# Kernel tuning notes

Hardware: AMD Instinct MI355X
Metric: run time of the kernel (lower is better)

Reference implementation:

```python
import jax, jax.numpy as jnp
import numpy as np

FEATURES = 64
GROUPS = 8
KH = KW = 3
PAD = 1


def conv2d(x, w):
    # x: [B,C,H,W], w: [O,I,kh,kw], stride 1, padding 1
    return jax.lax.conv_general_dilated(
        x, w, window_strides=(1, 1), padding=((PAD, PAD), (PAD, PAD)),
        dimension_numbers=('NCHW', 'OIHW', 'NCHW'))


def _bilinear_gather(x, ys, xs):
    # x: [B,C,H,W]; ys, xs: [B,K,H,W] float sample coords. Zero outside bounds
    # (torchvision deform_conv2d convention).
    B, C, H, W = x.shape
    xf = x.reshape(B, C, H * W)
    y0 = jnp.floor(ys)
    x0 = jnp.floor(xs)
    dy = ys - y0
    dx = xs - x0

    def corner(yi, xi, w):
        valid = (yi >= 0) & (yi < H) & (xi >= 0) & (xi < W)
        yc = jnp.clip(yi, 0, H - 1).astype(jnp.int32)
        xc = jnp.clip(xi, 0, W - 1).astype(jnp.int32)
        idx = (yc * W + xc).reshape(B, -1)  # [B, K*H*W]
        g = jax.vmap(lambda xb, ib: xb[:, ib])(xf, idx)  # [B,C,K*H*W]
        g = g.reshape(B, C, *ys.shape[1:])  # [B,C,K,H,W]
        wm = jnp.where(valid, w, 0.0).astype(x.dtype)[:, None]
        return g * wm

    return (corner(y0, x0, (1 - dy) * (1 - dx))
            + corner(y0, x0 + 1, (1 - dy) * dx)
            + corner(y0 + 1, x0, dy * (1 - dx))
            + corner(y0 + 1, x0 + 1, dy * dx))


def deform_conv2d(x, offset, weight, bias, groups):
    # x: [B,C,H,W]; offset: [B,2*K,H,W] as (dy,dx) pairs per kernel tap;
    # weight: [Cout, Cin//groups, KH, KW]; bias: [Cout]. stride=1, pad=1, dil=1.
    B, C, H, W = x.shape
    Cout = weight.shape[0]
    K = KH * KW
    ky, kx = jnp.meshgrid(jnp.arange(KH), jnp.arange(KW), indexing='ij')
    ky = ky.reshape(K).astype(x.dtype)
    kx = kx.reshape(K).astype(x.dtype)
    off = offset.reshape(B, K, 2, H, W)
    ys = ((jnp.arange(H, dtype=x.dtype) - PAD)[None, None, :, None]
          + ky[None, :, None, None] + off[:, :, 0])  # [B,K,H,W]
    xs = ((jnp.arange(W, dtype=x.dtype) - PAD)[None, None, None, :]
          + kx[None, :, None, None] + off[:, :, 1])
    patches = _bilinear_gather(x, ys, xs)  # [B,C,K,H,W]
    p = patches.reshape(B, groups, C // groups, K, H, W)
    wg = weight.reshape(groups, Cout // groups, C // groups, K)
    out = jnp.einsum('bgikhw,goik->bgohw', p, wg).reshape(B, Cout, H, W)
    return out + bias[None, :, None, None]


def setup_inputs() -> dict:
    key = jax.random.key(0)
    ks = jax.random.split(key, 7)
    C = FEATURES
    x = jax.random.normal(ks[0], (8, C, 128, 128), dtype=jnp.float32)
    fan = C * KH * KW
    offset_w = jax.random.normal(ks[1], (2 * KH * KW, C, KH, KW), jnp.float32) / np.sqrt(fan)
    offset_b = jax.random.normal(ks[2], (2 * KH * KW,), jnp.float32) * 0.01
    prelu_a = jnp.full((1,), 0.25, dtype=jnp.float32)
    deconv_w = jax.random.normal(ks[3], (C, C // GROUPS, KH, KW), jnp.float32) / np.sqrt((C // GROUPS) * KH * KW)
    deconv_b = jax.random.normal(ks[4], (C,), jnp.float32) * 0.01
    conv_w = jax.random.normal(ks[5], (C, C, KH, KW), jnp.float32) / np.sqrt(fan)
    return {"x": x, "offset_w": offset_w, "offset_b": offset_b,
            "prelu_a": prelu_a, "deconv_w": deconv_w, "deconv_b": deconv_b,
            "conv_w": conv_w}


def reference(x, offset_w, offset_b, prelu_a, deconv_w, deconv_b, conv_w):
    residual = x
    o = conv2d(x, offset_w) + offset_b[None, :, None, None]
    offset = jnp.where(o >= 0, o, prelu_a[0] * o)          # PReLU(offset_conv1(x))
    feat = deform_conv2d(x, offset, deconv_w, deconv_b, GROUPS)
    atten = jax.nn.softmax(conv2d(x, conv_w), axis=-1)     # softmax over W
    return atten * feat + residual
```

## Files before the change

### kernel.cpp

```cpp
#include <hip/hip_runtime.h>
#include <math.h>

#define BB 8
#define C 64
#define H 128
#define W 128
#define KO 18
#define NG 8
#define CPG 8
#define KK 9
#define HW (H * W)
#define NCO 96
#define KTOT 576
#define AROW 72
#define PROW 72

#define NB_XCL (BB * HW / 64)
#define NB_WT  (NCO * KTOT / 256)
#define NB_AWG (KK * 2 * 32 * 32 / 256)

typedef __bf16 bf16x8 __attribute__((ext_vector_type(8)));
typedef float f32x4 __attribute__((ext_vector_type(4)));
typedef unsigned int uint4v __attribute__((ext_vector_type(4)));

static __device__ __forceinline__ unsigned short f2bf(float f) {
    union { float f; unsigned u; } v; v.f = f;
    unsigned r = v.u + 0x7FFFu + ((v.u >> 16) & 1u);
    return (unsigned short)(r >> 16);
}

static __device__ __forceinline__ bf16x8 load_bf8(const unsigned short* p) {
    uint4v u = *(const uint4v*)p;
    return __builtin_bit_cast(bf16x8, u);
}
static __device__ __forceinline__ bf16x8 lds_bf8(const unsigned short* p) {
    uint4v u = *(const uint4v*)p;
    return __builtin_bit_cast(bf16x8, u);
}

static __device__ __forceinline__ float bflo(unsigned u) {
    union { unsigned u; float f; } v; v.u = u << 16; return v.f;
}
static __device__ __forceinline__ float bfhi(unsigned u) {
    union { unsigned u; float f; } v; v.u = u & 0xFFFF0000u; return v.f;
}

__global__ __launch_bounds__(256)
void prep_kernel(const float* __restrict__ x,
                 const float* __restrict__ convw,
                 const float* __restrict__ offw,
                 const float* __restrict__ dw,
                 unsigned short* __restrict__ xcl,
                 unsigned short* __restrict__ wT,
                 unsigned short* __restrict__ awg)
{
    const int blk = blockIdx.x;
    if (blk < NB_XCL) {
        const int lane = threadIdx.x & 63;
        const int cg = threadIdx.x >> 6;
        const size_t P = (size_t)blk * 64 + lane;
        const int b = (int)(P >> 14);
        const int hw = (int)(P & 16383);

        union { unsigned short s[16]; uint4v v[2]; } u;
        const float* xp = x + ((size_t)b * C + cg * 16) * HW + hw;
#pragma unroll
        for (int i = 0; i < 16; i++)
            u.s[i] = f2bf(xp[i * HW]);

        uint4v* dst = (uint4v*)(xcl + P * 64 + cg * 16);
        dst[0] = u.v[0];
        dst[1] = u.v[1];
    } else if (blk < NB_XCL + NB_WT) {
        const int i = (blk - NB_XCL) * 256 + threadIdx.x;
        const int k = i % KTOT;
        const int co = i / KTOT;
        const int t = k >> 6;
        const int ci = k & 63;
        float v = 0.f;
        if (co < 64)       v = convw[((size_t)co * C + ci) * KK + t];
        else if (co < 82)  v = offw[((size_t)(co - 64) * C + ci) * KK + t];
        wT[i] = f2bf(v);
    } else {
        const int i = (blk - NB_XCL - NB_WT) * 256 + threadIdx.x;
        const int ci = i & 31;
        const int row = (i >> 5) & 31;
        const int hf = (i >> 10) & 1;
        const int t = i >> 11;
        const int co = hf * 32 + row;
        const int cig = hf * 32 + ci;
        float v = 0.f;
        if ((co >> 3) == (cig >> 3))
            v = dw[((size_t)co * CPG + (cig & 7)) * KK + t];
        awg[i] = f2bf(v);
    }
}

static __device__ __forceinline__ void stage_tap(
    const unsigned short* __restrict__ wT, unsigned short* __restrict__ dst,
    int t, int tid)
{
#pragma unroll
    for (int c = tid; c < NCO * 8; c += 256) {
        const int row = c >> 3;
        const int col8 = (c & 7) * 8;
        *(uint4v*)(dst + row * AROW + col8) =
            *(const uint4v*)(wT + (size_t)row * KTOT + t * 64 + col8);
    }
}

static __device__ __forceinline__ void load_b(
    const unsigned short* __restrict__ xcl, int b, int h0, int col0, int qq,
    int t, bf16x8 (&dst)[2][4])
{
    const int dy = t / 3 - 1;
    const int dx = t % 3 - 1;
#pragma unroll
    for (int half = 0; half < 2; half++)
#pragma unroll
        for (int nt = 0; nt < 4; nt++) {
            const int y = h0 + (nt >> 1) + dy;
            const int xx = col0 + (nt & 1) * 16 + dx;
            const bool ok = (y >= 0) && (y < H) && (xx >= 0) && (xx < W);
            bf16x8 v = {};
            if (ok)
                v = load_bf8(xcl + (((size_t)(b * H + y) * W + xx) * 64
                                    + half * 32 + qq * 8));
            dst[half][nt] = v;
        }
}

__global__ __launch_bounds__(256, 2)
void conv_mfma_kernel(const unsigned short* __restrict__ xcl,
                      const unsigned short* __restrict__ wT,
                      const float* __restrict__ offb,
                      const float* __restrict__ prelu_a,
                      float* __restrict__ ws_offset,
                      float* __restrict__ ws_atten)
{
    __shared__ unsigned short aw[2][NCO * AROW];
    __shared__ float smax[4][2][64];
    __shared__ float ssum[4][2][64];

    const int lane = threadIdx.x & 63;
    const int q = __builtin_amdgcn_readfirstlane(threadIdx.x >> 6);
    const int m = lane & 15;
    const int qq = lane >> 4;
    const int hp = blockIdx.x & 63;
    const int b = blockIdx.x >> 6;
    const int h0 = hp * 2;

    f32x4 acc[4][6];
#pragma unroll
    for (int nt = 0; nt < 4; nt++)
#pragma unroll
        for (int mt = 0; mt < 6; mt++)
            acc[nt][mt] = (f32x4){0.f, 0.f, 0.f, 0.f};

    const int col0 = q * 32 + m;

    bf16x8 bcur[2][4], bnxt[2][4];
    stage_tap(wT, aw[0], 0, threadIdx.x);
    load_b(xcl, b, h0, col0, qq, 0, bcur);
    __syncthreads();

#pragma unroll
    for (int t = 0; t < KK; t++) {
        if (t + 1 < KK) {
            stage_tap(wT, aw[(t + 1) & 1], t + 1, threadIdx.x);
            load_b(xcl, b, h0, col0, qq, t + 1, bnxt);
        }

#pragma unroll
        for (int half = 0; half < 2; half++) {
#pragma unroll
            for (int mt = 0; mt < 6; mt++) {
                const bf16x8 afr = lds_bf8(
                    &aw[t & 1][(mt * 16 + m) * AROW + half * 32 + qq * 8]);
#pragma unroll
                for (int nt = 0; nt < 4; nt++)
                    acc[nt][mt] = __builtin_amdgcn_mfma_f32_16x16x32_bf16(
                        afr, bcur[half][nt], acc[nt][mt], 0, 0, 0);
            }
        }
        __syncthreads();

#pragma unroll
        for (int half = 0; half < 2; half++)
#pragma unroll
            for (int nt = 0; nt < 4; nt++)
                bcur[half][nt] = bnxt[half][nt];
    }

    const float a = prelu_a[0];
#pragma unroll
    for (int nt = 0; nt < 4; nt++) {
        const int wrow = h0 + (nt >> 1);
        const int wcol = col0 + (nt & 1) * 16;
#pragma unroll
        for (int r = 0; r < 4; r++) {
            const int j = qq * 4 + r;
            float v = acc[nt][4][r] + offb[j];
            v = (v >= 0.f) ? v : a * v;
            ws_offset[((size_t)(b * KO + j)) * HW + wrow * W + wcol] = v;
        }
#pragma unroll
        for (int r = 0; r < 4; r++) {
            const int j = 16 + qq * 4 + r;
            if (j < KO) {
                float v = acc[nt][5][r] + offb[j];
                v = (v >= 0.f) ? v : a * v;
                ws_offset[((size_t)(b * KO + j)) * HW + wrow * W + wcol] = v;
            }
        }
    }

    float pm[2][4][4];
#pragma unroll
    for (int rr = 0; rr < 2; rr++)
#pragma unroll
        for (int mt = 0; mt < 4; mt++)
#pragma unroll
            for (int r = 0; r < 4; r++)
                pm[rr][mt][r] = fmaxf(acc[rr * 2][mt][r], acc[rr * 2 + 1][mt][r]);
#pragma unroll
    for (int off = 1; off < 16; off <<= 1)
#pragma unroll
        for (int rr = 0; rr < 2; rr++)
#pragma unroll
            for (int mt = 0; mt < 4; mt++)
#pragma unroll
                for (int r = 0; r < 4; r++)
                    pm[rr][mt][r] = fmaxf(pm[rr][mt][r],
                                          __shfl_xor(pm[rr][mt][r], off, 64));
    if (m == 0) {
#pragma unroll
        for (int rr = 0; rr < 2; rr++)
#pragma unroll
            for (int mt = 0; mt < 4; mt++)
#pragma unroll
                for (int r = 0; r < 4; r++)
                    smax[q][rr][mt * 16 + qq * 4 + r] = pm[rr][mt][r];
    }
    __syncthreads();

    float gm[2][4][4];
#pragma unroll
    for (int rr = 0; rr < 2; rr++)
#pragma unroll
        for (int mt = 0; mt < 4; mt++)
#pragma unroll
            for (int r = 0; r < 4; r++) {
                const int co = mt * 16 + qq * 4 + r;
                gm[rr][mt][r] = fmaxf(fmaxf(smax[0][rr][co], smax[1][rr][co]),
                                      fmaxf(smax[2][rr][co], smax[3][rr][co]));
            }
    float ps[2][4][4];
#pragma unroll
    for (int rr = 0; rr < 2; rr++)
#pragma unroll
        for (int mt = 0; mt < 4; mt++)
#pragma unroll
            for (int r = 0; r < 4; r++) {
                acc[rr * 2][mt][r] = __expf(acc[rr * 2][mt][r] - gm[rr][mt][r]);
                acc[rr * 2 + 1][mt][r] = __expf(acc[rr * 2 + 1][mt][r] - gm[rr][mt][r]);
                ps[rr][mt][r] = acc[rr * 2][mt][r] + acc[rr * 2 + 1][mt][r];
            }
#pragma unroll
    for (int off = 1; off < 16; off <<= 1)
#pragma unroll
        for (int rr = 0; rr < 2; rr++)
#pragma unroll
            for (int mt = 0; mt < 4; mt++)
#pragma unroll
                for (int r = 0; r < 4; r++)
                    ps[rr][mt][r] += __shfl_xor(ps[rr][mt][r], off, 64);
    if (m == 0) {
#pragma unroll
        for (int rr = 0; rr < 2; rr++)
#pragma unroll
            for (int mt = 0; mt < 4; mt++)
#pragma unroll
                for (int r = 0; r < 4; r++)
                    ssum[q][rr][mt * 16 + qq * 4 + r] = ps[rr][mt][r];
    }
    __syncthreads();

#pragma unroll
    for (int rr = 0; rr < 2; rr++)
#pragma unroll
        for (int mt = 0; mt < 4; mt++)
#pragma unroll
            for (int r = 0; r < 4; r++) {
                const int co = mt * 16 + qq * 4 + r;
                const float rinv = 1.f / (ssum[0][rr][co] + ssum[1][rr][co]
                                          + ssum[2][rr][co] + ssum[3][rr][co]);
                float* op = ws_atten + ((size_t)(b * 64 + co)) * HW
                            + (h0 + rr) * W;
                op[col0] = acc[rr * 2][mt][r] * rinv;
                op[col0 + 16] = acc[rr * 2 + 1][mt][r] * rinv;
            }
}

__global__ __launch_bounds__(256)
void deform_mfma_kernel(const float* __restrict__ x,
                        const unsigned short* __restrict__ xcl,
                        const unsigned short* __restrict__ awg,
                        const float* __restrict__ db,
                        const float* __restrict__ ws_offset,
                        const float* __restrict__ ws_atten,
                        float* __restrict__ out)
{
    __shared__ unsigned short Pl[4 * 2 * 16 * PROW];

    const int lane = threadIdx.x & 63;
    const int wv = __builtin_amdgcn_readfirstlane(threadIdx.x >> 6);

    const int b = blockIdx.x & 7;
    const int h = (blockIdx.x >> 3) & 127;
    const int halfrow = blockIdx.x >> 10;
    const int w0 = halfrow * 64 + wv * 16;

    const int px = lane >> 2;
    const int ck = lane & 3;

    const unsigned short* xclb = xcl + (size_t)b * HW * 64;
    const float* offbase = ws_offset + (size_t)b * KO * HW + h * W + w0;
    unsigned short* const Pw0 = Pl + (wv * 2 + 0) * 16 * PROW;
    unsigned short* const Pw1 = Pl + (wv * 2 + 1) * 16 * PROW;

    f32x4 acc[4];
#pragma unroll
    for (int i = 0; i < 4; i++) acc[i] = (f32x4){0.f, 0.f, 0.f, 0.f};

    float dy = offbase[px];
    float dx = offbase[HW + px];

#pragma unroll
    for (int t = 0; t < KK; t++) {
        const int ky = t / 3;
        const int kx = t - ky * 3;

        float ndy = 0.f, ndx = 0.f;
        if (t + 1 < KK) {
            const float* ob2 = offbase + (size_t)(2 * t + 2) * HW;
            ndy = ob2[px];
            ndx = ob2[HW + px];
        }

        float wa[4];
        int oa[4];
        {
            const float ys = (float)(h - 1 + ky) + dy;
            const float xs = (float)(w0 + px - 1 + kx) + dx;
            const float y0f = floorf(ys), x0f = floorf(xs);
            const int y0 = (int)y0f, x0 = (int)x0f;
            const float fy = ys - y0f, fx = xs - x0f;
            const bool vy0 = (y0 >= 0) & (y0 < H), vy1 = (y0 + 1 >= 0) & (y0 + 1 < H);
            const bool vx0 = (x0 >= 0) & (x0 < W), vx1 = (x0 + 1 >= 0) & (x0 + 1 < W);
            wa[0] = (vy0 && vx0) ? (1.f - fy) * (1.f - fx) : 0.f;
            wa[1] = (vy0 && vx1) ? (1.f - fy) * fx : 0.f;
            wa[2] = (vy1 && vx0) ? fy * (1.f - fx) : 0.f;
            wa[3] = (vy1 && vx1) ? fy * fx : 0.f;
            const int yc0 = min(max(y0, 0), H - 1), yc1 = min(max(y0 + 1, 0), H - 1);
            const int xc0 = min(max(x0, 0), W - 1), xc1 = min(max(x0 + 1, 0), W - 1);
            oa[0] = (yc0 * W + xc0) * 64; oa[1] = (yc0 * W + xc1) * 64;
            oa[2] = (yc1 * W + xc0) * 64; oa[3] = (yc1 * W + xc1) * 64;
        }

        uint4v rA[4][2];
#pragma unroll
        for (int c = 0; c < 4; c++)
#pragma unroll
            for (int hh = 0; hh < 2; hh++)
                rA[c][hh] = *(const uint4v*)(xclb + oa[c] + ck * 16 + hh * 8);

        unsigned short* const Pwt = (t & 1) ? Pw1 : Pw0;

#pragma unroll
        for (int hh = 0; hh < 2; hh++) {
            bf16x8 pv;
#pragma unroll
            for (int d = 0; d < 4; d++) {
                const float lo = wa[0] * bflo(rA[0][hh][d]) + wa[1] * bflo(rA[1][hh][d])
                               + wa[2] * bflo(rA[2][hh][d]) + wa[3] * bflo(rA[3][hh][d]);
                const float hi = wa[0] * bfhi(rA[0][hh][d]) + wa[1] * bfhi(rA[1][hh][d])
                               + wa[2] * bfhi(rA[2][hh][d]) + wa[3] * bfhi(rA[3][hh][d]);
                pv[2 * d]     = (__bf16)lo;
                pv[2 * d + 1] = (__bf16)hi;
            }
            *(bf16x8*)(Pwt + px * PROW + ck * 16 + hh * 8) = pv;
        }

        asm volatile("s_waitcnt lgkmcnt(0)" ::: "memory");

        const int m = lane & 15;
        const int qq = lane >> 4;
#pragma unroll
        for (int hf = 0; hf < 2; hf++) {
            const bf16x8 bfr = lds_bf8(Pwt + m * PROW + hf * 32 + qq * 8);
#pragma unroll
            for (int mtl = 0; mtl < 2; mtl++) {
                const bf16x8 afr = load_bf8(
                    awg + ((size_t)((t * 2 + hf) * 32 + mtl * 16 + m)) * 32 + qq * 8);
                acc[hf * 2 + mtl] = __builtin_amdgcn_mfma_f32_16x16x32_bf16(
                    afr, bfr, acc[hf * 2 + mtl], 0, 0, 0);
            }
        }

        dy = ndy; dx = ndx;
    }

    const int n = lane & 15;
    const int qq = lane >> 4;
    const float* attp = ws_atten + (size_t)b * C * HW + h * W + w0 + n;
    const float* xr = x + (size_t)b * C * HW + h * W + w0 + n;
    float* op = out + (size_t)b * C * HW + h * W + w0 + n;
#pragma unroll
    for (int a = 0; a < 4; a++)
#pragma unroll
        for (int r = 0; r < 4; r++) {
            const int co = a * 16 + qq * 4 + r;
            const float f = acc[a][r] + db[co];
            op[(size_t)co * HW] = attp[(size_t)co * HW] * f + xr[(size_t)co * HW];
        }
}

extern "C" void kernel_launch(void* const* d_in, const int* in_sizes, int n_in,
                              void* d_out, int out_size, void* d_ws, size_t ws_size,
                              hipStream_t stream) {
    const float* x        = (const float*)d_in[0];
    const float* offset_w = (const float*)d_in[1];
    const float* offset_b = (const float*)d_in[2];
    const float* prelu_a  = (const float*)d_in[3];
    const float* deconv_w = (const float*)d_in[4];
    const float* deconv_b = (const float*)d_in[5];
    const float* conv_w   = (const float*)d_in[6];
    float* out = (float*)d_out;

    float* ws_offset = (float*)d_ws;
    float* ws_atten  = ws_offset + (size_t)BB * KO * HW;
    unsigned short* xcl = (unsigned short*)(ws_atten + (size_t)BB * C * HW);
    unsigned short* wT  = xcl + (size_t)BB * HW * C;
    unsigned short* awg = wT + (size_t)NCO * KTOT;

    prep_kernel<<<dim3(NB_XCL + NB_WT + NB_AWG), dim3(256), 0, stream>>>(
        x, conv_w, offset_w, deconv_w, xcl, wT, awg);

    conv_mfma_kernel<<<dim3(BB * H / 2), dim3(256), 0, stream>>>(
        xcl, wT, offset_b, prelu_a, ws_offset, ws_atten);

    deform_mfma_kernel<<<dim3(BB * H * 2), dim3(256), 0, stream>>>(
        x, xcl, awg, deconv_b, ws_offset, ws_atten, out);
}
```

Before: 180.0 us.

## Software-pipeline bilinear corner gathers one tap ahead with 8-lane channel mapping

```diff
diff --git a/kernel.cpp b/kernel.cpp
--- a/kernel.cpp
+++ b/kernel.cpp
@@ -43,6 +43,24 @@
 }
 static __device__ __forceinline__ float bfhi(unsigned u) {
     union { unsigned u; float f; } v; v.u = u & 0xFFFF0000u; return v.f;
+}
+
+static __device__ __forceinline__ void bilin_geom(
+    float ys, float xs, float* w4, int* o4)
+{
+    const float y0f = floorf(ys), x0f = floorf(xs);
+    const int y0 = (int)y0f, x0 = (int)x0f;
+    const float fy = ys - y0f, fx = xs - x0f;
+    const bool vy0 = (y0 >= 0) & (y0 < H), vy1 = (y0 + 1 >= 0) & (y0 + 1 < H);
+    const bool vx0 = (x0 >= 0) & (x0 < W), vx1 = (x0 + 1 >= 0) & (x0 + 1 < W);
+    w4[0] = (vy0 && vx0) ? (1.f - fy) * (1.f - fx) : 0.f;
+    w4[1] = (vy0 && vx1) ? (1.f - fy) * fx : 0.f;
+    w4[2] = (vy1 && vx0) ? fy * (1.f - fx) : 0.f;
+    w4[3] = (vy1 && vx1) ? fy * fx : 0.f;
+    const int yc0 = min(max(y0, 0), H - 1), yc1 = min(max(y0 + 1, 0), H - 1);
+    const int xc0 = min(max(x0, 0), W - 1), xc1 = min(max(x0 + 1, 0), W - 1);
+    o4[0] = (yc0 * W + xc0) * 64; o4[1] = (yc0 * W + xc1) * 64;
+    o4[2] = (yc1 * W + xc0) * 64; o4[3] = (yc1 * W + xc1) * 64;
 }
 
 __global__ __launch_bounds__(256)
@@ -321,8 +339,9 @@
     const int halfrow = blockIdx.x >> 10;
     const int w0 = halfrow * 64 + wv * 16;
 
-    const int px = lane >> 2;
-    const int ck = lane & 3;
+    const int pA = lane >> 3;
+    const int pB = pA + 8;
+    const int ch = lane & 7;
 
     const unsigned short* xclb = xcl + (size_t)b * HW * 64;
     const float* offbase = ws_offset + (size_t)b * KO * HW + h * W + w0;
@@ -333,63 +352,82 @@
 #pragma unroll
     for (int i = 0; i < 4; i++) acc[i] = (f32x4){0.f, 0.f, 0.f, 0.f};
 
-    float dy = offbase[px];
-    float dx = offbase[HW + px];
+    const float cdyA = offbase[pA];
+    const float cdxA = offbase[HW + pA];
+    const float cdyB = offbase[pB];
+    const float cdxB = offbase[HW + pB];
+    float ndyA = offbase[2 * HW + pA];
+    float ndxA = offbase[3 * HW + pA];
+    float ndyB = offbase[2 * HW + pB];
+    float ndxB = offbase[3 * HW + pB];
+
+    float waC[4], wbC[4];
+    int oaC[4], obC[4];
+    bilin_geom((float)(h - 1) + cdyA, (float)(w0 + pA - 1) + cdxA, waC, oaC);
+    bilin_geom((float)(h - 1) + cdyB, (float)(w0 + pB - 1) + cdxB, wbC, obC);
+    uint4v gA[4], gB[4];
+#pragma unroll
+    for (int c = 0; c < 4; c++) {
+        gA[c] = *(const uint4v*)(xclb + oaC[c] + ch * 8);
+        gB[c] = *(const uint4v*)(xclb + obC[c] + ch * 8);
+    }
 
 #pragma unroll
     for (int t = 0; t < KK; t++) {
-        const int ky = t / 3;
-        const int kx = t - ky * 3;
-
-        float ndy = 0.f, ndx = 0.f;
+        float n2dyA = 0.f, n2dxA = 0.f, n2dyB = 0.f, n2dxB = 0.f;
+        if (t + 2 < KK) {
+            const float* ob2 = offbase + (size_t)(2 * t + 4) * HW;
+            n2dyA = ob2[pA];
+            n2dxA = ob2[HW + pA];
+            n2dyB = ob2[pB];
+            n2dxB = ob2[HW + pB];
+        }
+
+        float waN[4], wbN[4];
+        uint4v gAN[4] = {}, gBN[4] = {};
+#pragma unroll
+        for (int c = 0; c < 4; c++) { waN[c] = 0.f; wbN[c] = 0.f; }
         if (t + 1 < KK) {
-            const float* ob2 = offbase + (size_t)(2 * t + 2) * HW;
-            ndy = ob2[px];
-            ndx = ob2[HW + px];
-        }
-
-        float wa[4];
-        int oa[4];
+            const int ky1 = (t + 1) / 3;
+            const int kx1 = (t + 1) - ky1 * 3;
+            int oaN[4], obN[4];
+            bilin_geom((float)(h - 1 + ky1) + ndyA,
+                       (float)(w0 + pA - 1 + kx1) + ndxA, waN, oaN);
+            bilin_geom((float)(h - 1 + ky1) + ndyB,
+                       (float)(w0 + pB - 1 + kx1) + ndxB, wbN, obN);
+#pragma unroll
+            for (int c = 0; c < 4; c++) {
+                gAN[c] = *(const uint4v*)(xclb + oaN[c] + ch * 8);
+                gBN[c] = *(const uint4v*)(xclb + obN[c] + ch * 8);
+            }
+        }
+
+        unsigned short* const Pwt = (t & 1) ? Pw1 : Pw0;
         {
-            const float ys = (float)(h - 1 + ky) + dy;
-            const float xs = (float)(w0 + px - 1 + kx) + dx;
-            const float y0f = floorf(ys), x0f = floorf(xs);
-            const int y0 = (int)y0f, x0 = (int)x0f;
-            const float fy = ys - y0f, fx = xs - x0f;
-            const bool vy0 = (y0 >= 0) & (y0 < H), vy1 = (y0 + 1 >= 0) & (y0 + 1 < H);
-            const bool vx0 = (x0 >= 0) & (x0 < W), vx1 = (x0 + 1 >= 0) & (x0 + 1 < W);
-            wa[0] = (vy0 && vx0) ? (1.f - fy) * (1.f - fx) : 0.f;
-            wa[1] = (vy0 && vx1) ? (1.f - fy) * fx : 0.f;
-            wa[2] = (vy1 && vx0) ? fy * (1.f - fx) : 0.f;
-            wa[3] = (vy1 && vx1) ? fy * fx : 0.f;
-            const int yc0 = min(max(y0, 0), H - 1), yc1 = min(max(y0 + 1, 0), H - 1);
-            const int xc0 = min(max(x0, 0), W - 1), xc1 = min(max(x0 + 1, 0), W - 1);
-            oa[0] = (yc0 * W + xc0) * 64; oa[1] = (yc0 * W + xc1) * 64;
-            oa[2] = (yc1 * W + xc0) * 64; oa[3] = (yc1 * W + xc1) * 64;
-        }
-
-        uint4v rA[4][2];
-#pragma unroll
-        for (int c = 0; c < 4; c++)
-#pragma unroll
-            for (int hh = 0; hh < 2; hh++)
-                rA[c][hh] = *(const uint4v*)(xclb + oa[c] + ck * 16 + hh * 8);
-
-        unsigned short* const Pwt = (t & 1) ? Pw1 : Pw0;
-
-#pragma unroll
-        for (int hh = 0; hh < 2; hh++) {
             bf16x8 pv;
 #pragma unroll
             for (int d = 0; d < 4; d++) {
-                const float lo = wa[0] * bflo(rA[0][hh][d]) + wa[1] * bflo(rA[1][hh][d])
-                               + wa[2] * bflo(rA[2][hh][d]) + wa[3] * bflo(rA[3][hh][d]);
-                const float hi = wa[0] * bfhi(rA[0][hh][d]) + wa[1] * bfhi(rA[1][hh][d])
-                               + wa[2] * bfhi(rA[2][hh][d]) + wa[3] * bfhi(rA[3][hh][d]);
+                const float lo = waC[0] * bflo(gA[0][d]) + waC[1] * bflo(gA[1][d])
+                               + waC[2] * bflo(gA[2][d]) + waC[3] * bflo(gA[3][d]);
+                const float hi = waC[0] * bfhi(gA[0][d]) + waC[1] * bfhi(gA[1][d])
+                               + waC[2] * bfhi(gA[2][d]) + waC[3] * bfhi(gA[3][d]);
                 pv[2 * d]     = (__bf16)lo;
                 pv[2 * d + 1] = (__bf16)hi;
             }
-            *(bf16x8*)(Pwt + px * PROW + ck * 16 + hh * 8) = pv;
+            *(bf16x8*)(Pwt + pA * PROW + ch * 8) = pv;
+        }
+        {
+            bf16x8 pv;
+#pragma unroll
+            for (int d = 0; d < 4; d++) {
+                const float lo = wbC[0] * bflo(gB[0][d]) + wbC[1] * bflo(gB[1][d])
+                               + wbC[2] * bflo(gB[2][d]) + wbC[3] * bflo(gB[3][d]);
+                const float hi = wbC[0] * bfhi(gB[0][d]) + wbC[1] * bfhi(gB[1][d])
+                               + wbC[2] * bfhi(gB[2][d]) + wbC[3] * bfhi(gB[3][d]);
+                pv[2 * d]     = (__bf16)lo;
+                pv[2 * d + 1] = (__bf16)hi;
+            }
+            *(bf16x8*)(Pwt + pB * PROW + ch * 8) = pv;
         }
 
         asm volatile("s_waitcnt lgkmcnt(0)" ::: "memory");
@@ -408,7 +446,12 @@
             }
         }
 
-        dy = ndy; dx = ndx;
+#pragma unroll
+        for (int c = 0; c < 4; c++) {
+            waC[c] = waN[c]; wbC[c] = wbN[c];
+            gA[c] = gAN[c]; gB[c] = gBN[c];
+        }
+        ndyA = n2dyA; ndxA = n2dxA; ndyB = n2dyB; ndxB = n2dxB;
     }
 
     const int n = lane & 15;
```

After: 177.2 us. No clear change (-1.6%).
